# Performance work log

Hardware: AMD Instinct MI355X
Metric: run time of the kernel (lower is better)

The kernel has to match this reference:

```python
import jax, jax.numpy as jnp
import numpy as np

N_NODES = 50000
N_EDGES = 800000
IN_FEATS = 256
HIDDEN = 128
HEADS = 2
NEG_SLOPE = 0.2


def gat_conv(x, edge_index, W, att_src, att_dst, bias, heads, out_c, concat):
    """PyG-style GATConv: linear -> per-edge attention logits -> segment
    softmax over destination neighborhoods -> scatter-add aggregate.
    Self-loops are added (PyG default add_self_loops=True)."""
    N = x.shape[0]
    h = (x @ W.T).reshape(N, heads, out_c)           # [N,H,C]
    loop = jnp.arange(N)
    src = jnp.concatenate([edge_index[0], loop])      # [E+N]
    dst = jnp.concatenate([edge_index[1], loop])
    a_src = jnp.sum(h * att_src, axis=-1)             # [N,H]
    a_dst = jnp.sum(h * att_dst, axis=-1)
    alpha = a_src[src] + a_dst[dst]                   # [E+N,H]
    alpha = jax.nn.leaky_relu(alpha, NEG_SLOPE)
    amax = jax.ops.segment_max(alpha, dst, num_segments=N)
    alpha = jnp.exp(alpha - amax[dst])
    denom = jax.ops.segment_sum(alpha, dst, num_segments=N)
    alpha = alpha / denom[dst]
    msg = h[src] * alpha[..., None]                   # [E+N,H,C]
    out = jax.ops.segment_sum(msg, dst, num_segments=N)  # [N,H,C]
    if concat:
        out = out.reshape(N, heads * out_c)
    else:
        out = out.mean(axis=1)
    return out + bias


def setup_inputs() -> dict:
    key = jax.random.key(0)
    ks = jax.random.split(key, 12)
    x = jax.random.normal(ks[0], (N_NODES, IN_FEATS), dtype=jnp.float32)
    edge_index = jax.random.randint(ks[1], (2, N_EDGES), 0, N_NODES, dtype=jnp.int64)
    s = 0.1
    W1 = jax.random.normal(ks[2], (HEADS * HIDDEN, IN_FEATS), dtype=jnp.float32) * s
    att_src1 = jax.random.normal(ks[3], (1, HEADS, HIDDEN), dtype=jnp.float32) * s
    att_dst1 = jax.random.normal(ks[4], (1, HEADS, HIDDEN), dtype=jnp.float32) * s
    b1 = jnp.zeros((HEADS * HIDDEN,), dtype=jnp.float32)
    W2 = jax.random.normal(ks[5], (HIDDEN, HEADS * HIDDEN), dtype=jnp.float32) * s
    att_src2 = jax.random.normal(ks[6], (1, 1, HIDDEN), dtype=jnp.float32) * s
    att_dst2 = jax.random.normal(ks[7], (1, 1, HIDDEN), dtype=jnp.float32) * s
    b2 = jnp.zeros((HIDDEN,), dtype=jnp.float32)
    return {"x": x, "edge_index": edge_index,
            "W1": W1, "att_src1": att_src1, "att_dst1": att_dst1, "b1": b1,
            "W2": W2, "att_src2": att_src2, "att_dst2": att_dst2, "b2": b2}


def reference(x, edge_index, W1, att_src1, att_dst1, b1, W2, att_src2, att_dst2, b2):
    h = gat_conv(x, edge_index, W1, att_src1, att_dst1, b1, HEADS, HIDDEN, True)
    h = jax.nn.relu(h)
    out = gat_conv(h, edge_index, W2, att_src2, att_dst2, b2, 1, HIDDEN, False)
    return out
```

## Files before the change

kernel.cpp:

```cpp
#include <hip/hip_runtime.h>
#include <hip/hip_bf16.h>


typedef _Float16 half8v __attribute__((ext_vector_type(8)));
typedef _Float16 half4v __attribute__((ext_vector_type(4)));
typedef _Float16 half2v __attribute__((ext_vector_type(2)));
typedef float f32x4 __attribute__((ext_vector_type(4)));


template <typename TA>
__global__ __launch_bounds__(256) void gemm_mfma_kernel(
    const TA* __restrict__ A,
    const float* __restrict__ B,
    _Float16* __restrict__ C,
    int M, int N, int K)
{
    constexpr int BM = 128, BK = 32, LDA = 40;
    __shared__ _Float16 Ah[BM * LDA];
    __shared__ _Float16 Bh[BM * LDA];

    const int tid = threadIdx.x;
    const int m0 = blockIdx.x * BM;
    const int n0 = blockIdx.y * BM;
    const int w  = tid >> 6;
    const int l  = tid & 63;
    const int wm = (w >> 1) * 64;
    const int wn = (w & 1) * 64;
    const int lr = l & 15;
    const int lq = l >> 4;

    f32x4 acc[4][4] = {};

    for (int k0 = 0; k0 < K; k0 += BK) {
        if constexpr (__is_same(TA, float)) {
#pragma unroll
            for (int it = 0; it < 4; ++it) {
                const int row = (tid >> 3) + it * 32;
                const int gm  = min(m0 + row, M - 1);
                const int c4  = (tid & 7) * 4;
                float4 v = *reinterpret_cast<const float4*>(A + (long)gm * K + k0 + c4);
                half4v o = { (_Float16)v.x, (_Float16)v.y, (_Float16)v.z, (_Float16)v.w };
                *reinterpret_cast<half4v*>(&Ah[row * LDA + c4]) = o;
            }
        } else {
#pragma unroll
            for (int it = 0; it < 2; ++it) {
                const int row = (tid >> 2) + it * 64;
                const int gm  = min(m0 + row, M - 1);
                const int c8  = (tid & 3) * 8;
                float4 v = *reinterpret_cast<const float4*>((const char*)A + ((long)gm * K + k0 + c8) * 2);
                *reinterpret_cast<float4*>(&Ah[row * LDA + c8]) = v;
            }
        }
#pragma unroll
        for (int it = 0; it < 4; ++it) {
            const int row = (tid >> 3) + it * 32;
            const int c4  = (tid & 7) * 4;
            float4 v = *reinterpret_cast<const float4*>(B + (long)(n0 + row) * K + k0 + c4);
            half4v o = { (_Float16)v.x, (_Float16)v.y, (_Float16)v.z, (_Float16)v.w };
            *reinterpret_cast<half4v*>(&Bh[row * LDA + c4]) = o;
        }
        __syncthreads();

        half8v af[4], bf[4];
#pragma unroll
        for (int i = 0; i < 4; ++i)
            af[i] = *reinterpret_cast<const half8v*>(&Ah[(wm + i * 16 + lr) * LDA + lq * 8]);
#pragma unroll
        for (int j = 0; j < 4; ++j)
            bf[j] = *reinterpret_cast<const half8v*>(&Bh[(wn + j * 16 + lr) * LDA + lq * 8]);
#pragma unroll
        for (int i = 0; i < 4; ++i)
#pragma unroll
            for (int j = 0; j < 4; ++j)
                acc[i][j] = __builtin_amdgcn_mfma_f32_16x16x32_f16(af[i], bf[j], acc[i][j], 0, 0, 0);
        __syncthreads();
    }

#pragma unroll
    for (int i = 0; i < 4; ++i) {
        const int gm_base = m0 + wm + i * 16 + lq * 4;
#pragma unroll
        for (int r = 0; r < 4; ++r) {
            const int gm = gm_base + r;
            if (gm < M) {
#pragma unroll
                for (int j = 0; j < 4; ++j) {
                    const int gn = n0 + wn + j * 16 + lr;
                    C[(long)gm * N + gn] = (_Float16)acc[i][j][r];
                }
            }
        }
    }
}


__global__ void count_kernel(const int* __restrict__ dst, int* __restrict__ deg, int E)
{
    const int e = blockIdx.x * blockDim.x + threadIdx.x;
    if (e < E) atomicAdd(&deg[dst[e]], 1);
}

__global__ __launch_bounds__(256) void block_scan_kernel(
    const int* __restrict__ deg, int* __restrict__ pre, int* __restrict__ blk, int n)
{
    __shared__ int s[256];
    const int t = threadIdx.x;
    const int base = blockIdx.x * 1024 + t * 4;
    int4 d = make_int4(-1, -1, -1, -1);
    if (base + 3 < n) d = *reinterpret_cast<const int4*>(deg + base);
    else {
        if (base + 0 < n) d.x = deg[base + 0];
        if (base + 1 < n) d.y = deg[base + 1];
        if (base + 2 < n) d.z = deg[base + 2];
        if (base + 3 < n) d.w = deg[base + 3];
    }
    const int v0 = d.x + 1, v1 = d.y + 1, v2 = d.z + 1, v3 = d.w + 1;
    s[t] = v0 + v1 + v2 + v3;
    __syncthreads();
#pragma unroll
    for (int o = 1; o < 256; o <<= 1) {
        int val = 0;
        if (t >= o) val = s[t - o];
        __syncthreads();
        s[t] += val;
        __syncthreads();
    }
    int run = (t == 0) ? 0 : s[t - 1];
    int4 o4;
    o4.x = run; run += v0;
    o4.y = run; run += v1;
    o4.z = run; run += v2;
    o4.w = run; run += v3;
    if (base + 3 < n) *reinterpret_cast<int4*>(pre + base) = o4;
    else {
        if (base + 0 < n) pre[base + 0] = o4.x;
        if (base + 1 < n) pre[base + 1] = o4.y;
        if (base + 2 < n) pre[base + 2] = o4.z;
        if (base + 3 < n) pre[base + 3] = o4.w;
    }
    if (t == 255) blk[blockIdx.x] = s[255];
}

__global__ void total_scan_kernel(const int* __restrict__ blk, int* __restrict__ blk_off,
                                  int* __restrict__ off_end, int nb)
{
    const int l = threadIdx.x;
    const int self = (l < nb) ? blk[l] : 0;
    int v = self;
#pragma unroll
    for (int o = 1; o < 64; o <<= 1) {
        int u = __shfl_up(v, o, 64);
        if (l >= o) v += u;
    }
    if (l < nb) blk_off[l] = v - self;
    if (l == nb - 1) *off_end = v;
}

__global__ __launch_bounds__(256) void finalize_scan_kernel(
    const int* __restrict__ pre, const int* __restrict__ blk_off,
    int* __restrict__ off, int* __restrict__ cursor, int n)
{
    const int t = threadIdx.x;
    const int base = blockIdx.x * 1024 + t * 4;
    const int add = blk_off[blockIdx.x];
    if (base + 3 < n) {
        int4 p = *reinterpret_cast<const int4*>(pre + base);
        p.x += add; p.y += add; p.z += add; p.w += add;
        *reinterpret_cast<int4*>(off + base) = p;
        *reinterpret_cast<int4*>(cursor + base) = p;
    } else {
#pragma unroll
        for (int k = 0; k < 4; ++k)
            if (base + k < n) {
                const int v = pre[base + k] + add;
                off[base + k] = v;
                cursor[base + k] = v;
            }
    }
}

__global__ void scatter_kernel(const int* __restrict__ src, const int* __restrict__ dst,
                               int* __restrict__ cursor, int* __restrict__ csr_src,
                               int E, int N)
{
    const int e = blockIdx.x * blockDim.x + threadIdx.x;
    if (e < E) {
        const int d = dst[e];
        const int p = atomicAdd(&cursor[d], 1);
        csr_src[p] = src[e];
    } else if (e < E + N) {
        const int nn = e - E;
        const int p = atomicAdd(&cursor[nn], 1);
        csr_src[p] = nn;
    }
}


template <int H>
__global__ __launch_bounds__(256) void att_kernel(
    const _Float16* __restrict__ h,
    const float* __restrict__ att_s,
    const float* __restrict__ att_d,
    float* __restrict__ a_s,
    float* __restrict__ a_d,
    int N)
{
    const int g = (blockIdx.x * 256 + threadIdx.x) >> 6;
    const int l = threadIdx.x & 63;
    if (g >= N * H) return;
    const int n  = g / H;
    const int hh = g % H;
    const _Float16* row = h + (long)n * (H * 128) + hh * 128;
    const float* asv = att_s + hh * 128;
    const float* adv = att_d + hh * 128;
    const float v0 = (float)row[l], v1 = (float)row[l + 64];
    float ss = v0 * asv[l] + v1 * asv[l + 64];
    float dd = v0 * adv[l] + v1 * adv[l + 64];
#pragma unroll
    for (int o = 32; o > 0; o >>= 1) {
        ss += __shfl_xor(ss, o, 64);
        dd += __shfl_xor(dd, o, 64);
    }
    if (l == 0) { a_s[g] = ss; a_d[g] = dd; }
}


#define AGG_TILE 64

template <int H, int C, int VPT, bool RELU, typename TOUT>
__global__ __launch_bounds__(H * C / VPT) void aggregate_kernel(
    const int* __restrict__ csr_off,
    const int* __restrict__ csr_src,
    const _Float16* __restrict__ h,
    const float* __restrict__ a_s,
    const float* __restrict__ a_d,
    const float* __restrict__ bias,
    TOUT* __restrict__ out)
{
    const int d   = blockIdx.x;
    const int t   = threadIdx.x;
    const int col = t * VPT;
    const int hh  = col / C;

    __shared__ int   s_src[AGG_TILE];
    __shared__ float s_w[AGG_TILE][H];

    const int beg = csr_off[d];
    const int end = csr_off[d + 1];

    float acc[VPT] = {};
    float wsum = 0.f;

    for (int base = beg; base < end; base += AGG_TILE) {
        const int len = min(AGG_TILE, end - base);
        if (t < len) {
            const int s = csr_src[base + t];
            s_src[t] = s;
#pragma unroll
            for (int h2 = 0; h2 < H; ++h2) {
                float logit = a_s[s * H + h2] + a_d[d * H + h2];
                logit = logit > 0.f ? logit : 0.2f * logit;
                s_w[t][h2] = __expf(logit);
            }
        }
        __syncthreads();
#pragma unroll 4
        for (int j = 0; j < len; ++j) {
            const float w = s_w[j][hh];
            const int   s = s_src[j];
            if constexpr (VPT == 4) {
                half4v hv = *reinterpret_cast<const half4v*>(h + (long)s * (H * C) + col);
                acc[0] += w * (float)hv.x;
                acc[1] += w * (float)hv.y;
                acc[2] += w * (float)hv.z;
                acc[3] += w * (float)hv.w;
            } else {
                half2v hv = *reinterpret_cast<const half2v*>(h + (long)s * (H * C) + col);
                acc[0] += w * (float)hv.x;
                acc[1] += w * (float)hv.y;
            }
            wsum += w;
        }
        __syncthreads();
    }

    const float inv = 1.f / wsum;
    float r[VPT];
#pragma unroll
    for (int k = 0; k < VPT; ++k) {
        r[k] = acc[k] * inv + bias[col + k];
        if (RELU) r[k] = r[k] > 0.f ? r[k] : 0.f;
    }
    if constexpr (__is_same(TOUT, _Float16)) {
#pragma unroll
        for (int k = 0; k < VPT; ++k)
            out[(long)d * (H * C) + col + k] = (_Float16)r[k];
    } else {
#pragma unroll
        for (int k = 0; k < VPT; ++k)
            out[(long)d * (H * C) + col + k] = r[k];
    }
}


extern "C" void kernel_launch(void* const* d_in, const int* in_sizes, int n_in,
                              void* d_out, int out_size, void* d_ws, size_t ws_size,
                              hipStream_t stream)
{
    const float* x    = (const float*)d_in[0];
    const int*   eidx = (const int*)d_in[1];
    const float* W1   = (const float*)d_in[2];
    const float* as1  = (const float*)d_in[3];
    const float* ad1  = (const float*)d_in[4];
    const float* b1   = (const float*)d_in[5];
    const float* W2   = (const float*)d_in[6];
    const float* as2  = (const float*)d_in[7];
    const float* ad2  = (const float*)d_in[8];
    const float* b2   = (const float*)d_in[9];
    float* out = (float*)d_out;

    const int IN_FEATS = 256;
    const int N = in_sizes[0] / IN_FEATS;
    const int E = in_sizes[1] / 2;

    const int* esrc = eidx;
    const int* edst = eidx + E;

    size_t off = 0;
    auto alloc = [&](size_t bytes) -> void* {
        void* p = (char*)d_ws + off;
        off += (bytes + 255) & ~(size_t)255;
        return p;
    };
    _Float16* h1h   = (_Float16*)alloc((size_t)N * 256 * 2);
    _Float16* o1h   = (_Float16*)alloc((size_t)N * 256 * 2);
    _Float16* h2h   = (_Float16*)alloc((size_t)N * 128 * 2);
    float* a1s      = (float*)alloc((size_t)N * 2 * 4);
    float* a1d      = (float*)alloc((size_t)N * 2 * 4);
    float* a2s      = (float*)alloc((size_t)N * 4);
    float* a2d      = (float*)alloc((size_t)N * 4);
    int*   deg      = (int*)alloc((size_t)N * 4);
    int*   pre      = (int*)alloc((size_t)N * 4);
    int*   cursor   = (int*)alloc((size_t)N * 4);
    int*   csr_off  = (int*)alloc((size_t)(N + 1) * 4);
    int*   csr_src  = (int*)alloc((size_t)(E + N) * 4);
    int*   blk      = (int*)alloc(64 * 4);
    int*   blk_off  = (int*)alloc(64 * 4);

    const int nbScan = (N + 1023) / 1024;

    hipMemsetAsync(deg, 0, (size_t)N * 4, stream);
    count_kernel<<<(E + 255) / 256, 256, 0, stream>>>(edst, deg, E);
    block_scan_kernel<<<nbScan, 256, 0, stream>>>(deg, pre, blk, N);
    total_scan_kernel<<<1, 64, 0, stream>>>(blk, blk_off, csr_off + N, nbScan);
    finalize_scan_kernel<<<nbScan, 256, 0, stream>>>(pre, blk_off, csr_off, cursor, N);
    scatter_kernel<<<(E + N + 255) / 256, 256, 0, stream>>>(esrc, edst, cursor, csr_src, E, N);

    {
        dim3 grid((N + 127) / 128, 256 / 128);
        gemm_mfma_kernel<float><<<grid, 256, 0, stream>>>(x, W1, h1h, N, 256, 256);
    }
    att_kernel<2><<<(N * 2 + 3) / 4, 256, 0, stream>>>(h1h, as1, ad1, a1s, a1d, N);
    aggregate_kernel<2, 128, 4, true, _Float16><<<N, 64, 0, stream>>>(
        csr_off, csr_src, h1h, a1s, a1d, b1, o1h);

    {
        dim3 grid((N + 127) / 128, 128 / 128);
        gemm_mfma_kernel<_Float16><<<grid, 256, 0, stream>>>(o1h, W2, h2h, N, 128, 256);
    }
    att_kernel<1><<<(N + 3) / 4, 256, 0, stream>>>(h2h, as2, ad2, a2s, a2d, N);
    aggregate_kernel<1, 128, 2, false, float><<<N, 64, 0, stream>>>(
        csr_off, csr_src, h2h, a2s, a2d, b2, out);
}
```

Baseline: 359.2 us.

## Fuse attention logits into GEMM epilogue and merge CSR build into cooperative kernel

```diff
diff --git a/kernel.cpp b/kernel.cpp
--- a/kernel.cpp
+++ b/kernel.cpp
@@ -1,5 +1,8 @@
 #include <hip/hip_runtime.h>
 #include <hip/hip_bf16.h>
+#include <hip/hip_cooperative_groups.h>
+
+namespace cg = cooperative_groups;
 
 
 typedef _Float16 half8v __attribute__((ext_vector_type(8)));
@@ -8,20 +11,27 @@
 typedef float f32x4 __attribute__((ext_vector_type(4)));
 
 
-template <typename TA>
-__global__ __launch_bounds__(256) void gemm_mfma_kernel(
+template <typename TA, int H>
+__global__ __launch_bounds__(256) void gemm_att_kernel(
     const TA* __restrict__ A,
     const float* __restrict__ B,
     _Float16* __restrict__ C,
-    int M, int N, int K)
+    const float* __restrict__ att_s,
+    const float* __restrict__ att_d,
+    float* __restrict__ a_s,
+    float* __restrict__ a_d,
+    int M, int K)
 {
     constexpr int BM = 128, BK = 32, LDA = 40;
+    constexpr int NCOL = H * 128;
     __shared__ _Float16 Ah[BM * LDA];
     __shared__ _Float16 Bh[BM * LDA];
+    __shared__ float red[2][2][64][2];
 
     const int tid = threadIdx.x;
     const int m0 = blockIdx.x * BM;
-    const int n0 = blockIdx.y * BM;
+    const int by = blockIdx.y;
+    const int n0 = by * 128;
     const int w  = tid >> 6;
     const int l  = tid & 63;
     const int wm = (w >> 1) * 64;
@@ -85,144 +95,184 @@
             const int gm = gm_base + r;
             if (gm < M) {
 #pragma unroll
-                for (int j = 0; j < 4; ++j) {
-                    const int gn = n0 + wn + j * 16 + lr;
-                    C[(long)gm * N + gn] = (_Float16)acc[i][j][r];
+                for (int j = 0; j < 4; ++j)
+                    C[(long)gm * NCOL + n0 + wn + j * 16 + lr] = (_Float16)acc[i][j][r];
+            }
+        }
+    }
+
+    float asv[4], adv[4];
+#pragma unroll
+    for (int j = 0; j < 4; ++j) {
+        asv[j] = att_s[n0 + wn + j * 16 + lr];
+        adv[j] = att_d[n0 + wn + j * 16 + lr];
+    }
+    float ps[4][4] = {}, pd[4][4] = {};
+#pragma unroll
+    for (int i = 0; i < 4; ++i)
+#pragma unroll
+        for (int j = 0; j < 4; ++j)
+#pragma unroll
+            for (int r = 0; r < 4; ++r) {
+                ps[i][r] += acc[i][j][r] * asv[j];
+                pd[i][r] += acc[i][j][r] * adv[j];
+            }
+#pragma unroll
+    for (int o = 1; o < 16; o <<= 1)
+#pragma unroll
+        for (int i = 0; i < 4; ++i)
+#pragma unroll
+            for (int r = 0; r < 4; ++r) {
+                ps[i][r] += __shfl_xor(ps[i][r], o, 64);
+                pd[i][r] += __shfl_xor(pd[i][r], o, 64);
+            }
+    if (lr == 0) {
+#pragma unroll
+        for (int i = 0; i < 4; ++i)
+#pragma unroll
+            for (int r = 0; r < 4; ++r) {
+                const int row = i * 16 + lq * 4 + r;
+                red[wm >> 6][wn >> 6][row][0] = ps[i][r];
+                red[wm >> 6][wn >> 6][row][1] = pd[i][r];
+            }
+    }
+    __syncthreads();
+    if (wn == 0) {
+        const int row = l;
+        const int gm = m0 + wm + row;
+        if (gm < M) {
+            const int wi = wm >> 6;
+            a_s[(long)gm * H + by] = red[wi][0][row][0] + red[wi][1][row][0];
+            a_d[(long)gm * H + by] = red[wi][0][row][1] + red[wi][1][row][1];
+        }
+    }
+}
+
+
+__global__ __launch_bounds__(256) void csr_build_kernel(
+    const int* __restrict__ src, const int* __restrict__ dst,
+    int* __restrict__ deg, int* __restrict__ pre,
+    int* __restrict__ blk, int* __restrict__ blk_off,
+    int* __restrict__ csr_off, int* __restrict__ cursor,
+    int* __restrict__ csr_src, int E, int N)
+{
+    cg::grid_group grid = cg::this_grid();
+    const int tid  = blockIdx.x * blockDim.x + threadIdx.x;
+    const int nthr = gridDim.x * blockDim.x;
+    const int t    = threadIdx.x;
+
+    for (int i = tid; i < N; i += nthr) deg[i] = 0;
+    grid.sync();
+
+    const int nq = (E + 3) / 4;
+    for (int q = tid; q < nq; q += nthr) {
+        const int e4 = q * 4;
+        if (e4 + 3 < E) {
+            const int4 d = *reinterpret_cast<const int4*>(dst + e4);
+            atomicAdd(&deg[d.x], 1);
+            atomicAdd(&deg[d.y], 1);
+            atomicAdd(&deg[d.z], 1);
+            atomicAdd(&deg[d.w], 1);
+        } else {
+            for (int k = e4; k < E; ++k) atomicAdd(&deg[dst[k]], 1);
+        }
+    }
+    grid.sync();
+
+    __shared__ int s[256];
+    const int nvb = (N + 1023) / 1024;
+    for (int vb = blockIdx.x; vb < nvb; vb += gridDim.x) {
+        const int base = vb * 1024 + t * 4;
+        int4 d = make_int4(-1, -1, -1, -1);
+        if (base + 3 < N) d = *reinterpret_cast<const int4*>(deg + base);
+        else {
+            if (base + 0 < N) d.x = deg[base + 0];
+            if (base + 1 < N) d.y = deg[base + 1];
+            if (base + 2 < N) d.z = deg[base + 2];
+            if (base + 3 < N) d.w = deg[base + 3];
+        }
+        const int v0 = d.x + 1, v1 = d.y + 1, v2 = d.z + 1, v3 = d.w + 1;
+        s[t] = v0 + v1 + v2 + v3;
+        __syncthreads();
+#pragma unroll
+        for (int o = 1; o < 256; o <<= 1) {
+            int val = 0;
+            if (t >= o) val = s[t - o];
+            __syncthreads();
+            s[t] += val;
+            __syncthreads();
+        }
+        int run = (t == 0) ? 0 : s[t - 1];
+        int4 o4;
+        o4.x = run; run += v0;
+        o4.y = run; run += v1;
+        o4.z = run; run += v2;
+        o4.w = run; run += v3;
+        if (base + 3 < N) *reinterpret_cast<int4*>(pre + base) = o4;
+        else {
+            if (base + 0 < N) pre[base + 0] = o4.x;
+            if (base + 1 < N) pre[base + 1] = o4.y;
+            if (base + 2 < N) pre[base + 2] = o4.z;
+            if (base + 3 < N) pre[base + 3] = o4.w;
+        }
+        if (t == 255) blk[vb] = s[255];
+        __syncthreads();
+    }
+    grid.sync();
+
+    if (blockIdx.x == 0 && t < 64) {
+        const int self = (t < nvb) ? blk[t] : 0;
+        int v = self;
+#pragma unroll
+        for (int o = 1; o < 64; o <<= 1) {
+            int u = __shfl_up(v, o, 64);
+            if (t >= o) v += u;
+        }
+        if (t < nvb) blk_off[t] = v - self;
+        if (t == nvb - 1) csr_off[N] = v;
+    }
+    grid.sync();
+
+    for (int vb = blockIdx.x; vb < nvb; vb += gridDim.x) {
+        const int base = vb * 1024 + t * 4;
+        const int add = blk_off[vb];
+        if (base + 3 < N) {
+            int4 p = *reinterpret_cast<const int4*>(pre + base);
+            p.x += add; p.y += add; p.z += add; p.w += add;
+            *reinterpret_cast<int4*>(csr_off + base) = p;
+            *reinterpret_cast<int4*>(cursor + base) = p;
+        } else {
+#pragma unroll
+            for (int k = 0; k < 4; ++k)
+                if (base + k < N) {
+                    const int v = pre[base + k] + add;
+                    csr_off[base + k] = v;
+                    cursor[base + k] = v;
                 }
-            }
-        }
-    }
-}
-
-
-__global__ void count_kernel(const int* __restrict__ dst, int* __restrict__ deg, int E)
-{
-    const int e = blockIdx.x * blockDim.x + threadIdx.x;
-    if (e < E) atomicAdd(&deg[dst[e]], 1);
-}
-
-__global__ __launch_bounds__(256) void block_scan_kernel(
-    const int* __restrict__ deg, int* __restrict__ pre, int* __restrict__ blk, int n)
-{
-    __shared__ int s[256];
-    const int t = threadIdx.x;
-    const int base = blockIdx.x * 1024 + t * 4;
-    int4 d = make_int4(-1, -1, -1, -1);
-    if (base + 3 < n) d = *reinterpret_cast<const int4*>(deg + base);
-    else {
-        if (base + 0 < n) d.x = deg[base + 0];
-        if (base + 1 < n) d.y = deg[base + 1];
-        if (base + 2 < n) d.z = deg[base + 2];
-        if (base + 3 < n) d.w = deg[base + 3];
-    }
-    const int v0 = d.x + 1, v1 = d.y + 1, v2 = d.z + 1, v3 = d.w + 1;
-    s[t] = v0 + v1 + v2 + v3;
-    __syncthreads();
-#pragma unroll
-    for (int o = 1; o < 256; o <<= 1) {
-        int val = 0;
-        if (t >= o) val = s[t - o];
-        __syncthreads();
-        s[t] += val;
-        __syncthreads();
-    }
-    int run = (t == 0) ? 0 : s[t - 1];
-    int4 o4;
-    o4.x = run; run += v0;
-    o4.y = run; run += v1;
-    o4.z = run; run += v2;
-    o4.w = run; run += v3;
-    if (base + 3 < n) *reinterpret_cast<int4*>(pre + base) = o4;
-    else {
-        if (base + 0 < n) pre[base + 0] = o4.x;
-        if (base + 1 < n) pre[base + 1] = o4.y;
-        if (base + 2 < n) pre[base + 2] = o4.z;
-        if (base + 3 < n) pre[base + 3] = o4.w;
-    }
-    if (t == 255) blk[blockIdx.x] = s[255];
-}
-
-__global__ void total_scan_kernel(const int* __restrict__ blk, int* __restrict__ blk_off,
-                                  int* __restrict__ off_end, int nb)
-{
-    const int l = threadIdx.x;
-    const int self = (l < nb) ? blk[l] : 0;
-    int v = self;
-#pragma unroll
-    for (int o = 1; o < 64; o <<= 1) {
-        int u = __shfl_up(v, o, 64);
-        if (l >= o) v += u;
-    }
-    if (l < nb) blk_off[l] = v - self;
-    if (l == nb - 1) *off_end = v;
-}
-
-__global__ __launch_bounds__(256) void finalize_scan_kernel(
-    const int* __restrict__ pre, const int* __restrict__ blk_off,
-    int* __restrict__ off, int* __restrict__ cursor, int n)
-{
-    const int t = threadIdx.x;
-    const int base = blockIdx.x * 1024 + t * 4;
-    const int add = blk_off[blockIdx.x];
-    if (base + 3 < n) {
-        int4 p = *reinterpret_cast<const int4*>(pre + base);
-        p.x += add; p.y += add; p.z += add; p.w += add;
-        *reinterpret_cast<int4*>(off + base) = p;
-        *reinterpret_cast<int4*>(cursor + base) = p;
-    } else {
-#pragma unroll
-        for (int k = 0; k < 4; ++k)
-            if (base + k < n) {
-                const int v = pre[base + k] + add;
-                off[base + k] = v;
-                cursor[base + k] = v;
-            }
-    }
-}
-
-__global__ void scatter_kernel(const int* __restrict__ src, const int* __restrict__ dst,
-                               int* __restrict__ cursor, int* __restrict__ csr_src,
-                               int E, int N)
-{
-    const int e = blockIdx.x * blockDim.x + threadIdx.x;
-    if (e < E) {
-        const int d = dst[e];
-        const int p = atomicAdd(&cursor[d], 1);
-        csr_src[p] = src[e];
-    } else if (e < E + N) {
-        const int nn = e - E;
-        const int p = atomicAdd(&cursor[nn], 1);
-        csr_src[p] = nn;
-    }
-}
-
-
-template <int H>
-__global__ __launch_bounds__(256) void att_kernel(
-    const _Float16* __restrict__ h,
-    const float* __restrict__ att_s,
-    const float* __restrict__ att_d,
-    float* __restrict__ a_s,
-    float* __restrict__ a_d,
-    int N)
-{
-    const int g = (blockIdx.x * 256 + threadIdx.x) >> 6;
-    const int l = threadIdx.x & 63;
-    if (g >= N * H) return;
-    const int n  = g / H;
-    const int hh = g % H;
-    const _Float16* row = h + (long)n * (H * 128) + hh * 128;
-    const float* asv = att_s + hh * 128;
-    const float* adv = att_d + hh * 128;
-    const float v0 = (float)row[l], v1 = (float)row[l + 64];
-    float ss = v0 * asv[l] + v1 * asv[l + 64];
-    float dd = v0 * adv[l] + v1 * adv[l + 64];
-#pragma unroll
-    for (int o = 32; o > 0; o >>= 1) {
-        ss += __shfl_xor(ss, o, 64);
-        dd += __shfl_xor(dd, o, 64);
-    }
-    if (l == 0) { a_s[g] = ss; a_d[g] = dd; }
+        }
+    }
+    grid.sync();
+
+    const int W = nq + N;
+    for (int wi = tid; wi < W; wi += nthr) {
+        if (wi < nq) {
+            const int e4 = wi * 4;
+            if (e4 + 3 < E) {
+                const int4 sv = *reinterpret_cast<const int4*>(src + e4);
+                const int4 dv = *reinterpret_cast<const int4*>(dst + e4);
+                csr_src[atomicAdd(&cursor[dv.x], 1)] = sv.x;
+                csr_src[atomicAdd(&cursor[dv.y], 1)] = sv.y;
+                csr_src[atomicAdd(&cursor[dv.z], 1)] = sv.z;
+                csr_src[atomicAdd(&cursor[dv.w], 1)] = sv.w;
+            } else {
+                for (int k = e4; k < E; ++k)
+                    csr_src[atomicAdd(&cursor[dst[k]], 1)] = src[k];
+            }
+        } else {
+            const int nn = wi - nq;
+            csr_src[atomicAdd(&cursor[nn], 1)] = nn;
+        }
+    }
 }
 
 
@@ -321,8 +371,8 @@
     float* out = (float*)d_out;
 
     const int IN_FEATS = 256;
-    const int N = in_sizes[0] / IN_FEATS;
-    const int E = in_sizes[1] / 2;
+    int N = in_sizes[0] / IN_FEATS;
+    int E = in_sizes[1] / 2;
 
     const int* esrc = eidx;
     const int* edst = eidx + E;
@@ -348,28 +398,27 @@
     int*   blk      = (int*)alloc(64 * 4);
     int*   blk_off  = (int*)alloc(64 * 4);
 
-    const int nbScan = (N + 1023) / 1024;
-
-    hipMemsetAsync(deg, 0, (size_t)N * 4, stream);
-    count_kernel<<<(E + 255) / 256, 256, 0, stream>>>(edst, deg, E);
-    block_scan_kernel<<<nbScan, 256, 0, stream>>>(deg, pre, blk, N);
-    total_scan_kernel<<<1, 64, 0, stream>>>(blk, blk_off, csr_off + N, nbScan);
-    finalize_scan_kernel<<<nbScan, 256, 0, stream>>>(pre, blk_off, csr_off, cursor, N);
-    scatter_kernel<<<(E + N + 255) / 256, 256, 0, stream>>>(esrc, edst, cursor, csr_src, E, N);
-
     {
-        dim3 grid((N + 127) / 128, 256 / 128);
-        gemm_mfma_kernel<float><<<grid, 256, 0, stream>>>(x, W1, h1h, N, 256, 256);
-    }
-    att_kernel<2><<<(N * 2 + 3) / 4, 256, 0, stream>>>(h1h, as1, ad1, a1s, a1d, N);
+        void* args[] = { (void*)&esrc, (void*)&edst, (void*)&deg, (void*)&pre,
+                         (void*)&blk, (void*)&blk_off, (void*)&csr_off,
+                         (void*)&cursor, (void*)&csr_src, (void*)&E, (void*)&N };
+        hipLaunchCooperativeKernel((void*)csr_build_kernel, dim3(256), dim3(256),
+                                   args, 0, stream);
+    }
+
+    {
+        dim3 grid((N + 127) / 128, 2);
+        gemm_att_kernel<float, 2><<<grid, 256, 0, stream>>>(
+            x, W1, h1h, as1, ad1, a1s, a1d, N, 256);
+    }
     aggregate_kernel<2, 128, 4, true, _Float16><<<N, 64, 0, stream>>>(
         csr_off, csr_src, h1h, a1s, a1d, b1, o1h);
 
     {
-        dim3 grid((N + 127) / 128, 128 / 128);
-        gemm_mfma_kernel<_Float16><<<grid, 256, 0, stream>>>(o1h, W2, h2h, N, 128, 256);
-    }
-    att_kernel<1><<<(N + 3) / 4, 256, 0, stream>>>(h2h, as2, ad2, a2s, a2d, N);
+        dim3 grid((N + 127) / 128, 1);
+        gemm_att_kernel<_Float16, 1><<<grid, 256, 0, stream>>>(
+            o1h, W2, h2h, as2, ad2, a2s, a2d, N, 256);
+    }
     aggregate_kernel<1, 128, 2, false, float><<<N, 64, 0, stream>>>(
         csr_off, csr_src, h2h, a2s, a2d, b2, out);
 }
```

Result: slower. 481.5 us (+34.1%).
